# Optimization experiments

Hardware: AMD Instinct MI355X
Metric: run time of the kernel (lower is better)

## Reference

```python
import jax, jax.numpy as jnp
import numpy as np

NUM_NODES_VOCAB = 1000000  # embedding table rows
N = 50000                  # nodes in this graph batch
E = 800000                 # edges (avg degree 16)
EMB = 128                  # embedding_dim
HID = 128                  # hidden_dim


def setup_inputs() -> dict:
    key = jax.random.key(0)
    ks = jax.random.split(key, 9)
    s_emb = 1.0 / np.sqrt(EMB)
    s_hid = 1.0 / np.sqrt(HID)
    return {
        "x": jax.random.randint(ks[0], (N,), 0, NUM_NODES_VOCAB),
        "edge_index": jax.random.randint(ks[1], (2, E), 0, N),
        "emb_table": jax.random.normal(ks[2], (NUM_NODES_VOCAB, EMB), jnp.float32),
        # SAGEConv layer 1: lin_l (neighbor agg, has bias), lin_r (root, no bias)
        "W1_l": jax.random.uniform(ks[3], (HID, EMB), jnp.float32, -s_emb, s_emb),
        "b1": jnp.zeros((HID,), jnp.float32),
        "W1_r": jax.random.uniform(ks[4], (HID, EMB), jnp.float32, -s_emb, s_emb),
        # SAGEConv layer 2
        "W2_l": jax.random.uniform(ks[5], (HID, HID), jnp.float32, -s_hid, s_hid),
        "b2": jnp.zeros((HID,), jnp.float32),
        "W2_r": jax.random.uniform(ks[6], (HID, HID), jnp.float32, -s_hid, s_hid),
    }


def _sage_conv(x, src, dst, W_l, b, W_r):
    # PyG SAGEConv (aggr='mean', root_weight=True):
    #   out = lin_l(mean_{j in N(i)} x_j) + lin_r(x_i)
    n = x.shape[0]
    msg = x[src]  # [E, d] gather
    agg = jax.ops.segment_sum(msg, dst, num_segments=n)  # [N, d]
    cnt = jax.ops.segment_sum(jnp.ones((src.shape[0],), x.dtype), dst, num_segments=n)
    agg = agg / jnp.maximum(cnt, 1.0)[:, None]
    return agg @ W_l.T + b + x @ W_r.T


def reference(x, edge_index, emb_table, W1_l, b1, W1_r, W2_l, b2, W2_r):
    src, dst = edge_index[0], edge_index[1]
    h = emb_table[x]  # [N, EMB] large-table lookup
    h = jax.nn.relu(_sage_conv(h, src, dst, W1_l, b1, W1_r))
    h = jax.nn.relu(_sage_conv(h, src, dst, W2_l, b2, W2_r))
    return h
```

## Files before the change

### kernel.cpp

```cpp
#include <hip/hip_runtime.h>
#include <stdint.h>

typedef short bf16x8 __attribute__((ext_vector_type(8)));
typedef float f32x4 __attribute__((ext_vector_type(4)));

__device__ __forceinline__ float bf2f(uint16_t u) {
  union { uint32_t i; float f; } v; v.i = ((uint32_t)u) << 16; return v.f;
}
__device__ __forceinline__ uint16_t f2bf(float f) {
  union { float f; uint32_t i; } v; v.f = f;
  uint32_t x = v.i;
  return (uint16_t)((x + 0x7fffu + ((x >> 16) & 1u)) >> 16);
}

__global__ void zero_kernel(int* cnt, int* cur, int* gcur, int n) {
  int i = blockIdx.x * 256 + threadIdx.x;
  if (i < n) { cnt[i] = 0; cur[i] = 0; }
  if (i == 0) *gcur = 0;
}

__global__ void count_kernel(const int* __restrict__ dst, int* __restrict__ cnt, int E) {
  int e = blockIdx.x * 256 + threadIdx.x;
  if (e < E) atomicAdd(&cnt[dst[e]], 1);
}

__global__ void alloc_kernel(const int* __restrict__ cnt, int* __restrict__ row_start,
                             int* __restrict__ gcur, int N) {
  int i = blockIdx.x * 256 + threadIdx.x;
  int lane = threadIdx.x & 63;
  int v = (i < N) ? cnt[i] : 0;
  int x = v;
#pragma unroll
  for (int off = 1; off < 64; off <<= 1) {
    int y = __shfl_up(x, off, 64);
    if (lane >= off) x += y;
  }
  int total = __shfl(x, 63, 64);
  int base = 0;
  if (lane == 63) base = atomicAdd(gcur, total);
  base = __shfl(base, 63, 64);
  if (i < N) row_start[i] = base + x - v;
}

__global__ void fill_kernel(const int* __restrict__ src, const int* __restrict__ dst,
                            const int* __restrict__ row_start, int* __restrict__ cur,
                            int* __restrict__ csr, int E) {
  int e = blockIdx.x * 256 + threadIdx.x;
  if (e < E) {
    int d = dst[e];
    int pos = row_start[d] + atomicAdd(&cur[d], 1);
    csr[pos] = src[e];
  }
}

__global__ void wcvt_kernel(const float* __restrict__ Wl1, const float* __restrict__ Wr1,
                            const float* __restrict__ Wl2, const float* __restrict__ Wr2,
                            uint32_t* __restrict__ Wcat) {
  int e = blockIdx.x * 256 + threadIdx.x;
  if (e >= 32768) return;
  int L = e >> 14, r = e & 16383;
  int o = r >> 7, kc = r & 127;
  const float* W = (kc < 64) ? (L ? Wl2 : Wl1) : (L ? Wr2 : Wr1);
  int k2 = (kc & 63) * 2;
  float a = W[o * 128 + k2];
  float b = W[o * 128 + k2 + 1];
  Wcat[e] = (uint32_t)f2bf(a) | ((uint32_t)f2bf(b) << 16);
}

__global__ void gather_kernel(const int* __restrict__ x, const float* __restrict__ emb,
                              uint32_t* __restrict__ A, int N) {
  int gw = (blockIdx.x * 256 + threadIdx.x) >> 6;
  int lane = threadIdx.x & 63;
  if (gw >= N) return;
  long row = x[gw];
  float2 v = *(const float2*)(emb + row * 128 + lane * 2);
  A[(long)gw * 128 + 64 + lane] = (uint32_t)f2bf(v.x) | ((uint32_t)f2bf(v.y) << 16);
}

__global__ void agg_kernel(uint32_t* __restrict__ A, const int* __restrict__ row_start,
                           const int* __restrict__ cnt, const int* __restrict__ csr, int N) {
  int gw = (blockIdx.x * 256 + threadIdx.x) >> 6;
  int lane = threadIdx.x & 63;
  if (gw >= N) return;
  int b = row_start[gw];
  int deg = cnt[gw];
  int e = b + deg;
  float ax = 0.f, ay = 0.f;
  int i = b;
  for (; i + 1 < e; i += 2) {
    int s0 = csr[i], s1 = csr[i + 1];
    uint32_t v0 = A[(long)s0 * 128 + 64 + lane];
    uint32_t v1 = A[(long)s1 * 128 + 64 + lane];
    ax += bf2f((uint16_t)(v0 & 0xffff)) + bf2f((uint16_t)(v1 & 0xffff));
    ay += bf2f((uint16_t)(v0 >> 16)) + bf2f((uint16_t)(v1 >> 16));
  }
  if (i < e) {
    uint32_t v = A[(long)csr[i] * 128 + 64 + lane];
    ax += bf2f((uint16_t)(v & 0xffff));
    ay += bf2f((uint16_t)(v >> 16));
  }
  float sc = 1.0f / (float)(deg > 0 ? deg : 1);
  A[(long)gw * 128 + lane] = (uint32_t)f2bf(ax * sc) | ((uint32_t)f2bf(ay * sc) << 16);
}

template <bool FINAL>
__global__ __launch_bounds__(256) void gemm_kernel(const uint16_t* __restrict__ A,
                                                   const uint32_t* __restrict__ Wcat,
                                                   const float* __restrict__ bias,
                                                   uint16_t* __restrict__ outH,
                                                   float* __restrict__ outF,
                                                   int N) {
  __shared__ uint32_t lds[16384];
  for (int e = threadIdx.x; e < 16384; e += 256) {
    int o = e >> 7, kc = e & 127;
    int g = kc >> 2, c = kc & 3;
    lds[(o << 7) | ((g ^ (o & 7)) << 2) | c] = Wcat[e];
  }
  __syncthreads();
  int lane = threadIdx.x & 63, wv = threadIdx.x >> 6;
  int wm = wv >> 1, wo = wv & 1;
  int ol = lane & 15, q = lane >> 4;
  int nb = blockIdx.x * 128 + wm * 64;
  f32x4 acc[4][4] = {};
#pragma unroll
  for (int ks = 0; ks < 8; ks++) {
    bf16x8 a[4], bfr[4];
#pragma unroll
    for (int mt = 0; mt < 4; mt++) {
      long n = nb + mt * 16 + ol;
      a[mt] = *(const bf16x8*)(A + n * 256 + ks * 32 + q * 8);
    }
#pragma unroll
    for (int ot = 0; ot < 4; ot++) {
      int o = wo * 64 + ot * 16 + ol;
      int g = ks * 4 + q;
      bfr[ot] = *(const bf16x8*)&lds[(o << 7) | ((g ^ (o & 7)) << 2)];
    }
#pragma unroll
    for (int mt = 0; mt < 4; mt++)
#pragma unroll
      for (int ot = 0; ot < 4; ot++)
        acc[mt][ot] = __builtin_amdgcn_mfma_f32_16x16x32_bf16(a[mt], bfr[ot], acc[mt][ot], 0, 0, 0);
  }
#pragma unroll
  for (int ot = 0; ot < 4; ot++) {
    int o = wo * 64 + ot * 16 + ol;
    float bv = bias[o];
#pragma unroll
    for (int mt = 0; mt < 4; mt++) {
#pragma unroll
      for (int r = 0; r < 4; r++) {
        int n = nb + mt * 16 + q * 4 + r;
        if (n < N) {
          float v = acc[mt][ot][r] + bv;
          v = v > 0.f ? v : 0.f;
          if (FINAL) outF[(long)n * 128 + o] = v;
          else outH[(long)n * 256 + 128 + o] = f2bf(v);
        }
      }
    }
  }
}

extern "C" void kernel_launch(void* const* d_in, const int* in_sizes, int n_in,
                              void* d_out, int out_size, void* d_ws, size_t ws_size,
                              hipStream_t stream) {
  const int* x = (const int*)d_in[0];
  const int* edge = (const int*)d_in[1];
  const float* emb = (const float*)d_in[2];
  const float* W1l = (const float*)d_in[3];
  const float* b1 = (const float*)d_in[4];
  const float* W1r = (const float*)d_in[5];
  const float* W2l = (const float*)d_in[6];
  const float* b2 = (const float*)d_in[7];
  const float* W2r = (const float*)d_in[8];
  const int N = in_sizes[0];
  const int E = in_sizes[1] / 2;
  const int* srcE = edge;
  const int* dstE = edge + E;

  const int Npad = ((N + 127) / 128) * 128;
  char* p = (char*)d_ws;
  uint16_t* A1 = (uint16_t*)p; p += (size_t)Npad * 256 * 2;
  uint16_t* A2 = (uint16_t*)p; p += (size_t)Npad * 256 * 2;
  uint32_t* Wcat = (uint32_t*)p; p += (size_t)2 * 16384 * 4;
  int* cnt = (int*)p;       p += (((size_t)N * 4 + 255) / 256) * 256;
  int* cur = (int*)p;       p += (((size_t)N * 4 + 255) / 256) * 256;
  int* row_start = (int*)p; p += (((size_t)N * 4 + 255) / 256) * 256;
  int* csr = (int*)p;       p += (((size_t)E * 4 + 255) / 256) * 256;
  int* gcur = (int*)p;      p += 256;

  zero_kernel<<<(N + 255) / 256, 256, 0, stream>>>(cnt, cur, gcur, N);
  count_kernel<<<(E + 255) / 256, 256, 0, stream>>>(dstE, cnt, E);
  alloc_kernel<<<(N + 255) / 256, 256, 0, stream>>>(cnt, row_start, gcur, N);
  fill_kernel<<<(E + 255) / 256, 256, 0, stream>>>(srcE, dstE, row_start, cur, csr, E);
  wcvt_kernel<<<128, 256, 0, stream>>>(W1l, W1r, W2l, W2r, Wcat);
  gather_kernel<<<(N + 3) / 4, 256, 0, stream>>>(x, emb, (uint32_t*)A1, N);
  agg_kernel<<<(N + 3) / 4, 256, 0, stream>>>((uint32_t*)A1, row_start, cnt, csr, N);
  gemm_kernel<false><<<Npad / 128, 256, 0, stream>>>(A1, Wcat, b1, A2, nullptr, N);
  agg_kernel<<<(N + 3) / 4, 256, 0, stream>>>((uint32_t*)A2, row_start, cnt, csr, N);
  gemm_kernel<true><<<Npad / 128, 256, 0, stream>>>(A2, Wcat + 16384, b2, nullptr, (float*)d_out, N);
}
```

Measured before the change: 808.2 us.

## Merge prep kernels into fewer launches and load neighbor indices cooperatively in aggregation

The zero and weight-conversion kernels are merged into one launch, and the edge-count and embedding-gather kernels into another, by splitting each grid into block ranges. This removes two launches and lets independent work share one grid. The aggregation kernel now loads up to 64 neighbor indices at once with one coalesced load per wavefront, broadcasts them with shuffles, and unrolls the gathers by four so more loads are in flight. The shuffle broadcasts add some instruction overhead.

```diff
diff --git a/kernel.cpp b/kernel.cpp
--- a/kernel.cpp
+++ b/kernel.cpp
@@ -13,15 +13,42 @@
   return (uint16_t)((x + 0x7fffu + ((x >> 16) & 1u)) >> 16);
 }
 
-__global__ void zero_kernel(int* cnt, int* cur, int* gcur, int n) {
-  int i = blockIdx.x * 256 + threadIdx.x;
-  if (i < n) { cnt[i] = 0; cur[i] = 0; }
-  if (i == 0) *gcur = 0;
-}
-
-__global__ void count_kernel(const int* __restrict__ dst, int* __restrict__ cnt, int E) {
-  int e = blockIdx.x * 256 + threadIdx.x;
-  if (e < E) atomicAdd(&cnt[dst[e]], 1);
+__global__ void prep0_kernel(int* __restrict__ cnt, int* __restrict__ cur, int* __restrict__ gcur,
+                             int N, int zb,
+                             const float* __restrict__ Wl1, const float* __restrict__ Wr1,
+                             const float* __restrict__ Wl2, const float* __restrict__ Wr2,
+                             uint32_t* __restrict__ Wcat) {
+  if ((int)blockIdx.x < zb) {
+    int i = blockIdx.x * 256 + threadIdx.x;
+    if (i < N) { cnt[i] = 0; cur[i] = 0; }
+    if (i == 0 && blockIdx.x == 0) *gcur = 0;
+  } else {
+    int e = (blockIdx.x - zb) * 256 + threadIdx.x;
+    if (e >= 32768) return;
+    int L = e >> 14, r = e & 16383;
+    int o = r >> 7, kc = r & 127;
+    const float* W = (kc < 64) ? (L ? Wl2 : Wl1) : (L ? Wr2 : Wr1);
+    int k2 = (kc & 63) * 2;
+    float a = W[o * 128 + k2];
+    float b = W[o * 128 + k2 + 1];
+    Wcat[e] = (uint32_t)f2bf(a) | ((uint32_t)f2bf(b) << 16);
+  }
+}
+
+__global__ void count_gather_kernel(const int* __restrict__ dst, int* __restrict__ cnt, int E, int cb,
+                                    const int* __restrict__ x, const float* __restrict__ emb,
+                                    uint32_t* __restrict__ A, int N) {
+  if ((int)blockIdx.x < cb) {
+    int e = blockIdx.x * 256 + threadIdx.x;
+    if (e < E) atomicAdd(&cnt[dst[e]], 1);
+  } else {
+    int gw = ((blockIdx.x - cb) * 256 + threadIdx.x) >> 6;
+    int lane = threadIdx.x & 63;
+    if (gw >= N) return;
+    long row = x[gw];
+    float2 v = *(const float2*)(emb + row * 128 + lane * 2);
+    A[(long)gw * 128 + 64 + lane] = (uint32_t)f2bf(v.x) | ((uint32_t)f2bf(v.y) << 16);
+  }
 }
 
 __global__ void alloc_kernel(const int* __restrict__ cnt, int* __restrict__ row_start,
@@ -53,30 +80,6 @@
   }
 }
 
-__global__ void wcvt_kernel(const float* __restrict__ Wl1, const float* __restrict__ Wr1,
-                            const float* __restrict__ Wl2, const float* __restrict__ Wr2,
-                            uint32_t* __restrict__ Wcat) {
-  int e = blockIdx.x * 256 + threadIdx.x;
-  if (e >= 32768) return;
-  int L = e >> 14, r = e & 16383;
-  int o = r >> 7, kc = r & 127;
-  const float* W = (kc < 64) ? (L ? Wl2 : Wl1) : (L ? Wr2 : Wr1);
-  int k2 = (kc & 63) * 2;
-  float a = W[o * 128 + k2];
-  float b = W[o * 128 + k2 + 1];
-  Wcat[e] = (uint32_t)f2bf(a) | ((uint32_t)f2bf(b) << 16);
-}
-
-__global__ void gather_kernel(const int* __restrict__ x, const float* __restrict__ emb,
-                              uint32_t* __restrict__ A, int N) {
-  int gw = (blockIdx.x * 256 + threadIdx.x) >> 6;
-  int lane = threadIdx.x & 63;
-  if (gw >= N) return;
-  long row = x[gw];
-  float2 v = *(const float2*)(emb + row * 128 + lane * 2);
-  A[(long)gw * 128 + 64 + lane] = (uint32_t)f2bf(v.x) | ((uint32_t)f2bf(v.y) << 16);
-}
-
 __global__ void agg_kernel(uint32_t* __restrict__ A, const int* __restrict__ row_start,
                            const int* __restrict__ cnt, const int* __restrict__ csr, int N) {
   int gw = (blockIdx.x * 256 + threadIdx.x) >> 6;
@@ -84,20 +87,42 @@
   if (gw >= N) return;
   int b = row_start[gw];
   int deg = cnt[gw];
-  int e = b + deg;
   float ax = 0.f, ay = 0.f;
-  int i = b;
-  for (; i + 1 < e; i += 2) {
-    int s0 = csr[i], s1 = csr[i + 1];
-    uint32_t v0 = A[(long)s0 * 128 + 64 + lane];
-    uint32_t v1 = A[(long)s1 * 128 + 64 + lane];
-    ax += bf2f((uint16_t)(v0 & 0xffff)) + bf2f((uint16_t)(v1 & 0xffff));
-    ay += bf2f((uint16_t)(v0 >> 16)) + bf2f((uint16_t)(v1 >> 16));
-  }
-  if (i < e) {
-    uint32_t v = A[(long)csr[i] * 128 + 64 + lane];
-    ax += bf2f((uint16_t)(v & 0xffff));
-    ay += bf2f((uint16_t)(v >> 16));
+  int done = 0;
+  while (done < deg) {
+    int chunk = deg - done;
+    if (chunk > 64) chunk = 64;
+    int idx = (lane < chunk) ? csr[b + done + lane] : 0;
+    int i = 0;
+    for (; i + 3 < chunk; i += 4) {
+      int s0 = __shfl(idx, i, 64);
+      int s1 = __shfl(idx, i + 1, 64);
+      int s2 = __shfl(idx, i + 2, 64);
+      int s3 = __shfl(idx, i + 3, 64);
+      uint32_t v0 = A[(long)s0 * 128 + 64 + lane];
+      uint32_t v1 = A[(long)s1 * 128 + 64 + lane];
+      uint32_t v2 = A[(long)s2 * 128 + 64 + lane];
+      uint32_t v3 = A[(long)s3 * 128 + 64 + lane];
+      ax += bf2f((uint16_t)(v0 & 0xffff)) + bf2f((uint16_t)(v1 & 0xffff));
+      ay += bf2f((uint16_t)(v0 >> 16)) + bf2f((uint16_t)(v1 >> 16));
+      ax += bf2f((uint16_t)(v2 & 0xffff)) + bf2f((uint16_t)(v3 & 0xffff));
+      ay += bf2f((uint16_t)(v2 >> 16)) + bf2f((uint16_t)(v3 >> 16));
+    }
+    for (; i + 1 < chunk; i += 2) {
+      int s0 = __shfl(idx, i, 64);
+      int s1 = __shfl(idx, i + 1, 64);
+      uint32_t v0 = A[(long)s0 * 128 + 64 + lane];
+      uint32_t v1 = A[(long)s1 * 128 + 64 + lane];
+      ax += bf2f((uint16_t)(v0 & 0xffff)) + bf2f((uint16_t)(v1 & 0xffff));
+      ay += bf2f((uint16_t)(v0 >> 16)) + bf2f((uint16_t)(v1 >> 16));
+    }
+    if (i < chunk) {
+      int s0 = __shfl(idx, i, 64);
+      uint32_t v = A[(long)s0 * 128 + 64 + lane];
+      ax += bf2f((uint16_t)(v & 0xffff));
+      ay += bf2f((uint16_t)(v >> 16));
+    }
+    done += chunk;
   }
   float sc = 1.0f / (float)(deg > 0 ? deg : 1);
   A[(long)gw * 128 + lane] = (uint32_t)f2bf(ax * sc) | ((uint32_t)f2bf(ay * sc) << 16);
@@ -190,12 +215,14 @@
   int* csr = (int*)p;       p += (((size_t)E * 4 + 255) / 256) * 256;
   int* gcur = (int*)p;      p += 256;
 
-  zero_kernel<<<(N + 255) / 256, 256, 0, stream>>>(cnt, cur, gcur, N);
-  count_kernel<<<(E + 255) / 256, 256, 0, stream>>>(dstE, cnt, E);
+  const int zb = (N + 255) / 256;
+  const int cb = (E + 255) / 256;
+  const int gb = (N + 3) / 4;
+
+  prep0_kernel<<<zb + 128, 256, 0, stream>>>(cnt, cur, gcur, N, zb, W1l, W1r, W2l, W2r, Wcat);
+  count_gather_kernel<<<cb + gb, 256, 0, stream>>>(dstE, cnt, E, cb, x, emb, (uint32_t*)A1, N);
   alloc_kernel<<<(N + 255) / 256, 256, 0, stream>>>(cnt, row_start, gcur, N);
   fill_kernel<<<(E + 255) / 256, 256, 0, stream>>>(srcE, dstE, row_start, cur, csr, E);
-  wcvt_kernel<<<128, 256, 0, stream>>>(W1l, W1r, W2l, W2r, Wcat);
-  gather_kernel<<<(N + 3) / 4, 256, 0, stream>>>(x, emb, (uint32_t*)A1, N);
   agg_kernel<<<(N + 3) / 4, 256, 0, stream>>>((uint32_t*)A1, row_start, cnt, csr, N);
   gemm_kernel<false><<<Npad / 128, 256, 0, stream>>>(A1, Wcat, b1, A2, nullptr, N);
   agg_kernel<<<(N + 3) / 4, 256, 0, stream>>>((uint32_t*)A2, row_start, cnt, csr, N);
```

Measured after the change: 765.5 us. -5.3%, faster.
